# Optimization experiments

Hardware: AMD Instinct MI355X
Metric: run time of the kernel (lower is better)

The kernel has to match this reference:

```python
import jax, jax.numpy as jnp
import numpy as np

B, S, DIM = 2, 2048, 1024
H, DH = 16, 64
WIN = 512


def setup_inputs() -> dict:
    key = jax.random.key(0)
    k1, k2, k3 = jax.random.split(key, 3)
    x = jax.random.normal(k1, (B, S, DIM), dtype=jnp.float32)
    Wqkv = jax.random.normal(k2, (DIM, 3 * H * DH), dtype=jnp.float32) * (DIM ** -0.5)
    Wout = jax.random.normal(k3, (H * DH, DIM), dtype=jnp.float32) * ((H * DH) ** -0.5)
    return {"x": x, "Wqkv": Wqkv, "Wout": Wout}


def reference(x, Wqkv, Wout):
    b, s, _ = x.shape
    qkv = jnp.einsum('bsd,de->bse', x, Wqkv)  # (B,S,3*H*DH)
    q, k, v = jnp.split(qkv, 3, axis=-1)
    # -> (B,H,S,DH)
    q = q.reshape(b, s, H, DH).transpose(0, 2, 1, 3)
    k = k.reshape(b, s, H, DH).transpose(0, 2, 1, 3)
    v = v.reshape(b, s, H, DH).transpose(0, 2, 1, 3)
    scale = DH ** -0.5  # attention sees per-head dim
    scores = jnp.einsum('bhsd,bhtd->bhst', q, k) * scale  # dense (B,H,S,S)
    i = jnp.arange(s)[:, None]
    j = jnp.arange(s)[None, :]
    mask = (j >= i - WIN + 1) & (j <= i)  # causal sliding window
    mask_value = -jnp.finfo(scores.dtype).max
    scores = jnp.where(mask[None, None], scores, mask_value)
    attn = jax.nn.softmax(scores, axis=-1)
    out = jnp.einsum('bhst,bhtd->bhsd', attn, v)
    out = out.transpose(0, 2, 1, 3).reshape(b, s, H * DH)
    return jnp.einsum('bse,ed->bsd', out, Wout)
```

## Files before the change

kernel.cpp:

```cpp
#include <hip/hip_runtime.h>

#define S_LEN 2048
#define BATCH 2
#define HDIM 1024
#define NH 16
#define DH 64
#define WINSZ 512
#define MROWS (BATCH * S_LEN)

typedef __attribute__((ext_vector_type(8))) short bfrag;
typedef __attribute__((ext_vector_type(4))) float f32x4;
typedef __attribute__((ext_vector_type(4))) int i128;

__device__ __forceinline__ short f2bf(float f) {
    union { float f; unsigned u; } v;
    v.f = f;
    unsigned r = v.u + 0x7fffu + ((v.u >> 16) & 1u);
    return (short)(r >> 16);
}

__device__ __forceinline__ void gload_lds16(const short* g, short* l) {
    __builtin_amdgcn_global_load_lds(
        (const __attribute__((address_space(1))) unsigned int*)g,
        (__attribute__((address_space(3))) unsigned int*)l, 16, 0, 0);
}

__global__ __launch_bounds__(256)
void prep_kernel(const float* __restrict__ x, const float* __restrict__ Wqkv,
                 const float* __restrict__ Wout,
                 short* __restrict__ x_bf, short* __restrict__ wqkv_t, short* __restrict__ wout_t)
{
    __shared__ float tile[32][33];
    const int bid = blockIdx.x;
    const int t = threadIdx.x;

    if (bid < 4096) {
        int i = bid * 256 + t;
        float4 v = ((const float4*)x)[i];
        union { short s[4]; int2 p; } u;
        u.s[0] = f2bf(v.x); u.s[1] = f2bf(v.y); u.s[2] = f2bf(v.z); u.s[3] = f2bf(v.w);
        ((int2*)x_bf)[i] = u.p;
        return;
    }

    const float* in;
    short* out;
    int R, C, bx, by;
    if (bid < 7168) {
        int lb = bid - 4096;
        in = Wqkv; out = wqkv_t; R = 1024; C = 3072;
        bx = lb % 96; by = lb / 96;
    } else {
        int lb = bid - 7168;
        in = Wout; out = wout_t; R = 1024; C = 1024;
        bx = lb & 31; by = lb >> 5;
    }
    int tc0 = bx * 32, tr0 = by * 32;
    int c = t & 31, r0 = t >> 5;
    #pragma unroll
    for (int k = 0; k < 4; ++k) {
        int r = r0 + k * 8;
        tile[r][c] = in[(size_t)(tr0 + r) * C + tc0 + c];
    }
    __syncthreads();
    int r2 = t & 31, c0 = t >> 5;
    #pragma unroll
    for (int k = 0; k < 4; ++k) {
        int c2 = c0 + k * 8;
        out[(size_t)(tc0 + c2) * R + tr0 + r2] = f2bf(tile[r2][c2]);
    }
}

__global__ __launch_bounds__(256, 2)
void gemm_qkv(const short* __restrict__ A, const short* __restrict__ Bt,
              short* __restrict__ qk_rm, short* __restrict__ vto)
{
    __shared__ __align__(16) short smraw[17408];
    short (*Al)[4096] = (short(*)[4096])smraw;
    short (*Bl)[4096] = (short(*)[4096])(smraw + 8192);
    const int K = HDIM;
    const int t = threadIdx.x;
    const int lane = t & 63;
    const int wave = t >> 6;
    const int wr = wave >> 1, wc = wave & 1;
    const int m0 = blockIdx.y * 128, n0 = blockIdx.x * 128;
    const int lq = lane & 15;
    const int g = lane >> 4;
    const int lk8 = g << 3;

    f32x4 acc[4][4];
    #pragma unroll
    for (int m = 0; m < 4; ++m)
        #pragma unroll
        for (int n = 0; n < 4; ++n)
            acc[m][n] = (f32x4){0.f, 0.f, 0.f, 0.f};

    const int row0s = t >> 2, col0s = (t & 3) << 3;
    const int row1s = (256 + t) >> 2;
    const size_t dst0 = (size_t)(wave * 64) * 8;
    const size_t dst1 = (size_t)(256 + wave * 64) * 8;

    auto stage = [&](int k0, int sb) {
        gload_lds16(&A[(size_t)(m0 + row0s) * K + k0 + col0s], &Al[sb][0] + dst0);
        gload_lds16(&Bt[(size_t)(n0 + row0s) * K + k0 + col0s], &Bl[sb][0] + dst0);
        gload_lds16(&A[(size_t)(m0 + row1s) * K + k0 + col0s], &Al[sb][0] + dst1);
        gload_lds16(&Bt[(size_t)(n0 + row1s) * K + k0 + col0s], &Bl[sb][0] + dst1);
    };

    const int nk = K >> 5;
    stage(0, 0);
    __syncthreads();
    for (int ki = 0; ki < nk; ++ki) {
        const int cur = ki & 1;
        if (ki + 1 < nk) stage((ki + 1) << 5, cur ^ 1);
        bfrag af[4], bfr[4];
        #pragma unroll
        for (int m = 0; m < 4; ++m)
            af[m] = *(const bfrag*)(&Al[cur][(wr * 64 + m * 16 + lq) * 32 + lk8]);
        #pragma unroll
        for (int n = 0; n < 4; ++n)
            bfr[n] = *(const bfrag*)(&Bl[cur][(wc * 64 + n * 16 + lq) * 32 + lk8]);
        #pragma unroll
        for (int m = 0; m < 4; ++m)
            #pragma unroll
            for (int n = 0; n < 4; ++n)
                acc[m][n] = __builtin_amdgcn_mfma_f32_16x16x32_bf16(af[m], bfr[n], acc[m][n], 0, 0, 0);
        __syncthreads();
    }

    if (n0 < 2048) {
        #pragma unroll
        for (int m = 0; m < 4; ++m)
            #pragma unroll
            for (int n = 0; n < 4; ++n) {
                int col = n0 + wc * 64 + n * 16 + lq;
                int row0 = m0 + wr * 64 + m * 16 + g * 4;
                #pragma unroll
                for (int r = 0; r < 4; ++r)
                    qk_rm[(size_t)(row0 + r) * 2048 + col] = f2bf(acc[m][n][r]);
            }
    } else {
        short* T = smraw;
        #pragma unroll
        for (int m = 0; m < 4; ++m)
            #pragma unroll
            for (int n = 0; n < 4; ++n) {
                int cl = wc * 64 + n * 16 + lq;
                int rl0 = wr * 64 + m * 16 + g * 4;
                union { short sh[4]; int2 w; } u;
                #pragma unroll
                for (int r = 0; r < 4; ++r) u.sh[r] = f2bf(acc[m][n][r]);
                *(int2*)(&T[cl * 136 + rl0]) = u.w;
            }
        __syncthreads();
        const int b = m0 >> 11, sbase = m0 & 2047;
        const int h0 = (n0 - 2048) >> 6;
        #pragma unroll
        for (int i = 0; i < 8; ++i) {
            int c2 = i * 256 + t;
            int rv = c2 >> 4;
            int sc = (c2 & 15) << 3;
            int h = h0 + (rv >> 6), dh = rv & 63;
            i128 v = *(const i128*)(&T[rv * 136 + sc]);
            *(i128*)(&vto[((size_t)((b * NH + h) * DH + dh)) * S_LEN + sbase + sc]) = v;
        }
    }
}

__global__ __launch_bounds__(256, 2)
void gemm_out(const short* __restrict__ A, const short* __restrict__ Bt,
              float* __restrict__ co)
{
    __shared__ __align__(16) short Al[2][128 * 32];
    __shared__ __align__(16) short Bl[2][128 * 32];
    const int K = HDIM, N = HDIM;
    const int t = threadIdx.x;
    const int lane = t & 63;
    const int wave = t >> 6;
    const int wr = wave >> 1, wc = wave & 1;
    const int m0 = blockIdx.y * 128, n0 = blockIdx.x * 128;
    const int lq = lane & 15;
    const int g = lane >> 4;
    const int lk8 = g << 3;

    f32x4 acc[4][4];
    #pragma unroll
    for (int m = 0; m < 4; ++m)
        #pragma unroll
        for (int n = 0; n < 4; ++n)
            acc[m][n] = (f32x4){0.f, 0.f, 0.f, 0.f};

    const int row0s = t >> 2, col0s = (t & 3) << 3;
    const int row1s = (256 + t) >> 2;
    const size_t dst0 = (size_t)(wave * 64) * 8;
    const size_t dst1 = (size_t)(256 + wave * 64) * 8;

    auto stage = [&](int k0, int sb) {
        gload_lds16(&A[(size_t)(m0 + row0s) * K + k0 + col0s], &Al[sb][0] + dst0);
        gload_lds16(&Bt[(size_t)(n0 + row0s) * K + k0 + col0s], &Bl[sb][0] + dst0);
        gload_lds16(&A[(size_t)(m0 + row1s) * K + k0 + col0s], &Al[sb][0] + dst1);
        gload_lds16(&Bt[(size_t)(n0 + row1s) * K + k0 + col0s], &Bl[sb][0] + dst1);
    };

    const int nk = K >> 5;
    stage(0, 0);
    __syncthreads();
    for (int ki = 0; ki < nk; ++ki) {
        const int cur = ki & 1;
        if (ki + 1 < nk) stage((ki + 1) << 5, cur ^ 1);
        bfrag af[4], bfr[4];
        #pragma unroll
        for (int m = 0; m < 4; ++m)
            af[m] = *(const bfrag*)(&Al[cur][(wr * 64 + m * 16 + lq) * 32 + lk8]);
        #pragma unroll
        for (int n = 0; n < 4; ++n)
            bfr[n] = *(const bfrag*)(&Bl[cur][(wc * 64 + n * 16 + lq) * 32 + lk8]);
        #pragma unroll
        for (int m = 0; m < 4; ++m)
            #pragma unroll
            for (int n = 0; n < 4; ++n)
                acc[m][n] = __builtin_amdgcn_mfma_f32_16x16x32_bf16(af[m], bfr[n], acc[m][n], 0, 0, 0);
        __syncthreads();
    }

    #pragma unroll
    for (int m = 0; m < 4; ++m)
        #pragma unroll
        for (int n = 0; n < 4; ++n) {
            int col = n0 + wc * 64 + n * 16 + lq;
            int row0 = m0 + wr * 64 + m * 16 + g * 4;
            #pragma unroll
            for (int r = 0; r < 4; ++r)
                co[(size_t)(row0 + r) * N + col] = acc[m][n][r];
        }
}

__global__ __launch_bounds__(256, 4)
void attn_kernel(const short* __restrict__ qk, const short* __restrict__ vt,
                 short* __restrict__ attno)
{
    __shared__ __align__(16) short Kl[2][64 * 64];
    __shared__ __align__(16) short Vl[2][64 * 64];
    __shared__ __align__(16) short Pl[4][16 * 64];

    const int bid = blockIdx.x;
    const int logical = (bid & 7) * 128 + (bid >> 3);
    const int qblk = logical & 31;
    const int bh = logical >> 5;
    const int b = bh >> 4, h = bh & 15;

    const int t = threadIdx.x;
    const int wave = t >> 6, lane = t & 63;
    const int qb0 = qblk * 64;
    const int i0 = qb0 + wave * 16;
    const short* qbase = qk + (size_t)b * S_LEN * 2048 + h * 64;
    const short* kbase = qk + (size_t)b * S_LEN * 2048 + 1024 + h * 64;
    const short* vp = vt + (size_t)bh * DH * S_LEN;
    char* myP = (char*)&Pl[wave][0];

    const int lq = lane & 15;
    const int g = lane >> 4;
    const int swz = (lq & 7) << 4;
    const int l7 = lq & 7;

    bfrag qf[2];
    qf[0] = *(const bfrag*)(&qbase[(size_t)(i0 + lq) * 2048 + (g << 3)]);
    qf[1] = *(const bfrag*)(&qbase[(size_t)(i0 + lq) * 2048 + 32 + (g << 3)]);

    f32x4 oacc[4];
    #pragma unroll
    for (int d = 0; d < 4; ++d) oacc[d] = (f32x4){0.f, 0.f, 0.f, 0.f};
    float m2 = -1e30f, lrun = 0.f;
    const float QSCALE = 0.125f * 1.44269504f;
    const int qi = i0 + lq;

    int j_lo = qb0 - (WINSZ - 1);
    if (j_lo < 0) j_lo = 0;
    j_lo &= ~63;
    const int nT = ((qb0 + 64) - j_lo) >> 6;

    auto stage = [&](int j0, short* kbuf, short* vbuf) {
        #pragma unroll
        for (int qq = 0; qq < 2; ++qq) {
            int chunk = qq * 256 + wave * 64 + lane;
            int row = chunk >> 3;
            int cc = (chunk & 7) ^ (row & 7);
            short* kdst = kbuf + (size_t)(qq * 256 + wave * 64) * 8;
            short* vdst = vbuf + (size_t)(qq * 256 + wave * 64) * 8;
            gload_lds16(kbase + (size_t)(j_lo + j0 + row) * 2048 + cc * 8, kdst);
            gload_lds16(vp + (size_t)row * S_LEN + j_lo + j0 + cc * 8, vdst);
        }
    };

    stage(0, Kl[0], Vl[0]);
    __syncthreads();

    for (int ti = 0; ti < nT; ++ti) {
        const int cur = ti & 1;
        const int j0 = j_lo + ti * 64;
        if (ti + 1 < nT) stage((ti + 1) * 64, Kl[cur ^ 1], Vl[cur ^ 1]);

        const short* Kc = Kl[cur];
        const short* Vc = Vl[cur];

        f32x4 sc[4];
        __builtin_amdgcn_s_setprio(1);
        #pragma unroll
        for (int tc = 0; tc < 4; ++tc) {
            bfrag a0 = *(const bfrag*)(&Kc[(tc * 16 + lq) * 64 + ((g ^ l7) << 3)]);
            bfrag a1 = *(const bfrag*)(&Kc[(tc * 16 + lq) * 64 + (((4 | g) ^ l7) << 3)]);
            f32x4 z = (f32x4){0.f, 0.f, 0.f, 0.f};
            z = __builtin_amdgcn_mfma_f32_16x16x32_bf16(a0, qf[0], z, 0, 0, 0);
            z = __builtin_amdgcn_mfma_f32_16x16x32_bf16(a1, qf[1], z, 0, 0, 0);
            sc[tc] = z;
        }
        __builtin_amdgcn_s_setprio(0);

        const bool nomask = (j0 >= i0 - (WINSZ - 16)) && (j0 + 63 <= i0);
        float s[4][4];
        float pm = -1e30f;
        #pragma unroll
        for (int tc = 0; tc < 4; ++tc)
            #pragma unroll
            for (int r = 0; r < 4; ++r) {
                float sv = sc[tc][r] * QSCALE;
                if (!nomask) {
                    int kj = j0 + tc * 16 + 4 * g + r;
                    sv = ((kj <= qi) && (kj > qi - WINSZ)) ? sv : -1e30f;
                }
                s[tc][r] = sv;
                pm = fmaxf(pm, sv);
            }
        pm = fmaxf(pm, __shfl_xor(pm, 16));
        pm = fmaxf(pm, __shfl_xor(pm, 32));
        float mnew = fmaxf(m2, pm);
        float scale_old = exp2f(m2 - mnew);
        m2 = mnew;
        float p[4][4];
        float rs = 0.f;
        #pragma unroll
        for (int tc = 0; tc < 4; ++tc)
            #pragma unroll
            for (int r = 0; r < 4; ++r) {
                p[tc][r] = exp2f(s[tc][r] - mnew);
                rs += p[tc][r];
            }
        rs += __shfl_xor(rs, 16);
        rs += __shfl_xor(rs, 32);
        lrun = lrun * scale_old + rs;
        #pragma unroll
        for (int d = 0; d < 4; ++d) {
            f32x4 o = oacc[d];
            o[0] *= scale_old; o[1] *= scale_old; o[2] *= scale_old; o[3] *= scale_old;
            oacc[d] = o;
        }

        #pragma unroll
        for (int tc = 0; tc < 4; ++tc) {
            union { short sh[4]; int2 w; } u;
            u.sh[0] = f2bf(p[tc][0]); u.sh[1] = f2bf(p[tc][1]);
            u.sh[2] = f2bf(p[tc][2]); u.sh[3] = f2bf(p[tc][3]);
            int wb = (lq * 128 + tc * 32 + g * 8) ^ swz;
            *(int2*)(myP + wb) = u.w;
        }
        asm volatile("s_waitcnt lgkmcnt(0)" ::: "memory");

        __builtin_amdgcn_s_setprio(1);
        #pragma unroll
        for (int kt = 0; kt < 2; ++kt) {
            int rb = (lq * 128 + kt * 64 + g * 16) ^ swz;
            bfrag pf = *(const bfrag*)(myP + rb);
            #pragma unroll
            for (int d = 0; d < 4; ++d) {
                bfrag vfr = *(const bfrag*)(&Vc[(d * 16 + lq) * 64 + (((kt * 4 + g) ^ l7) << 3)]);
                oacc[d] = __builtin_amdgcn_mfma_f32_16x16x32_bf16(vfr, pf, oacc[d], 0, 0, 0);
            }
        }
        __builtin_amdgcn_s_setprio(0);
        __syncthreads();
    }

    const float inv_l = 1.f / lrun;
    size_t rowbase = ((size_t)(b * S_LEN + qi)) * HDIM + h * DH;
    #pragma unroll
    for (int d = 0; d < 4; ++d) {
        union { short sh[4]; int2 w; } u;
        #pragma unroll
        for (int r = 0; r < 4; ++r)
            u.sh[r] = f2bf(oacc[d][r] * inv_l);
        *(int2*)(&attno[rowbase + d * 16 + 4 * g]) = u.w;
    }
}

extern "C" void kernel_launch(void* const* d_in, const int* in_sizes, int n_in,
                              void* d_out, int out_size, void* d_ws, size_t ws_size,
                              hipStream_t stream) {
    const float* x = (const float*)d_in[0];
    const float* Wqkv = (const float*)d_in[1];
    const float* Wout = (const float*)d_in[2];
    float* out = (float*)d_out;
    char* ws = (char*)d_ws;

    short* x_bf   = (short*)(ws);
    short* wqkv_t = (short*)(ws + 8388608);
    short* wout_t = (short*)(ws + 14680064);
    short* qk_rm  = (short*)(ws + 16777216);
    short* v_t    = (short*)(ws + 33554432);
    short* attno  = x_bf;

    prep_kernel<<<8192, 256, 0, stream>>>(x, Wqkv, Wout, x_bf, wqkv_t, wout_t);
    gemm_qkv<<<dim3(24, 32), 256, 0, stream>>>(x_bf, wqkv_t, qk_rm, v_t);
    attn_kernel<<<dim3(BATCH * NH * (S_LEN / 64)), 256, 0, stream>>>(qk_rm, v_t, attno);
    gemm_out<<<dim3(8, 32), 256, 0, stream>>>(attno, wout_t, out);
}
```

Measured before the change: 166.6 us.

## Double attention query tile, deepen gemm_out K-step, pack transpose stores

The attention kernel now gives each wave 32 query rows (128 per block), so every staged K/V tile is reused across twice as many queries. The block count halves, occupancy is retuned to 3, and the P buffer doubles. gemm_out stages 64-wide K slices to halve the barrier iterations. The weight transpose writes two bf16 values per 32-bit store, and gemm_qkv launch bounds are raised to 3. The trade-offs are more registers and LDS per block and fewer blocks to fill the GPU.

```diff
diff --git a/kernel.cpp b/kernel.cpp
--- a/kernel.cpp
+++ b/kernel.cpp
@@ -63,15 +63,18 @@
         tile[r][c] = in[(size_t)(tr0 + r) * C + tc0 + c];
     }
     __syncthreads();
-    int r2 = t & 31, c0 = t >> 5;
-    #pragma unroll
-    for (int k = 0; k < 4; ++k) {
-        int c2 = c0 + k * 8;
-        out[(size_t)(tc0 + c2) * R + tr0 + r2] = f2bf(tile[r2][c2]);
-    }
-}
-
-__global__ __launch_bounds__(256, 2)
+    int r2p = (t & 15) << 1, c0 = t >> 4;
+    #pragma unroll
+    for (int k = 0; k < 2; ++k) {
+        int c2 = c0 + k * 16;
+        union { short sh[2]; int w; } u;
+        u.sh[0] = f2bf(tile[r2p][c2]);
+        u.sh[1] = f2bf(tile[r2p + 1][c2]);
+        *(int*)(&out[(size_t)(tc0 + c2) * R + tr0 + r2p]) = u.w;
+    }
+}
+
+__global__ __launch_bounds__(256, 3)
 void gemm_qkv(const short* __restrict__ A, const short* __restrict__ Bt,
               short* __restrict__ qk_rm, short* __restrict__ vto)
 {
@@ -171,8 +174,8 @@
 void gemm_out(const short* __restrict__ A, const short* __restrict__ Bt,
               float* __restrict__ co)
 {
-    __shared__ __align__(16) short Al[2][128 * 32];
-    __shared__ __align__(16) short Bl[2][128 * 32];
+    __shared__ __align__(16) short Al[2][128 * 64];
+    __shared__ __align__(16) short Bl[2][128 * 64];
     const int K = HDIM, N = HDIM;
     const int t = threadIdx.x;
     const int lane = t & 63;
@@ -181,7 +184,6 @@
     const int m0 = blockIdx.y * 128, n0 = blockIdx.x * 128;
     const int lq = lane & 15;
     const int g = lane >> 4;
-    const int lk8 = g << 3;
 
     f32x4 acc[4][4];
     #pragma unroll
@@ -190,36 +192,41 @@
         for (int n = 0; n < 4; ++n)
             acc[m][n] = (f32x4){0.f, 0.f, 0.f, 0.f};
 
-    const int row0s = t >> 2, col0s = (t & 3) << 3;
-    const int row1s = (256 + t) >> 2;
-    const size_t dst0 = (size_t)(wave * 64) * 8;
-    const size_t dst1 = (size_t)(256 + wave * 64) * 8;
-
     auto stage = [&](int k0, int sb) {
-        gload_lds16(&A[(size_t)(m0 + row0s) * K + k0 + col0s], &Al[sb][0] + dst0);
-        gload_lds16(&Bt[(size_t)(n0 + row0s) * K + k0 + col0s], &Bl[sb][0] + dst0);
-        gload_lds16(&A[(size_t)(m0 + row1s) * K + k0 + col0s], &Al[sb][0] + dst1);
-        gload_lds16(&Bt[(size_t)(n0 + row1s) * K + k0 + col0s], &Bl[sb][0] + dst1);
+        #pragma unroll
+        for (int q = 0; q < 4; ++q) {
+            int chunk = q * 256 + t;
+            int row = chunk >> 3, col = (chunk & 7) << 3;
+            size_t dst = (size_t)(q * 256 + wave * 64) * 8;
+            gload_lds16(&A[(size_t)(m0 + row) * K + k0 + col], &Al[sb][0] + dst);
+            gload_lds16(&Bt[(size_t)(n0 + row) * K + k0 + col], &Bl[sb][0] + dst);
+        }
     };
 
-    const int nk = K >> 5;
+    const int nk = K >> 6;
     stage(0, 0);
     __syncthreads();
     for (int ki = 0; ki < nk; ++ki) {
         const int cur = ki & 1;
-        if (ki + 1 < nk) stage((ki + 1) << 5, cur ^ 1);
-        bfrag af[4], bfr[4];
-        #pragma unroll
-        for (int m = 0; m < 4; ++m)
-            af[m] = *(const bfrag*)(&Al[cur][(wr * 64 + m * 16 + lq) * 32 + lk8]);
+        if (ki + 1 < nk) stage((ki + 1) << 6, cur ^ 1);
+        bfrag af[4][2], bfr[4][2];
+        #pragma unroll
+        for (int m = 0; m < 4; ++m)
+            #pragma unroll
+            for (int ks = 0; ks < 2; ++ks)
+                af[m][ks] = *(const bfrag*)(&Al[cur][(wr * 64 + m * 16 + lq) * 64 + ks * 32 + (g << 3)]);
         #pragma unroll
         for (int n = 0; n < 4; ++n)
-            bfr[n] = *(const bfrag*)(&Bl[cur][(wc * 64 + n * 16 + lq) * 32 + lk8]);
-        #pragma unroll
-        for (int m = 0; m < 4; ++m)
-            #pragma unroll
-            for (int n = 0; n < 4; ++n)
-                acc[m][n] = __builtin_amdgcn_mfma_f32_16x16x32_bf16(af[m], bfr[n], acc[m][n], 0, 0, 0);
+            #pragma unroll
+            for (int ks = 0; ks < 2; ++ks)
+                bfr[n][ks] = *(const bfrag*)(&Bl[cur][(wc * 64 + n * 16 + lq) * 64 + ks * 32 + (g << 3)]);
+        #pragma unroll
+        for (int m = 0; m < 4; ++m)
+            #pragma unroll
+            for (int n = 0; n < 4; ++n) {
+                acc[m][n] = __builtin_amdgcn_mfma_f32_16x16x32_bf16(af[m][0], bfr[n][0], acc[m][n], 0, 0, 0);
+                acc[m][n] = __builtin_amdgcn_mfma_f32_16x16x32_bf16(af[m][1], bfr[n][1], acc[m][n], 0, 0, 0);
+            }
         __syncthreads();
     }
 
@@ -235,24 +242,24 @@
         }
 }
 
-__global__ __launch_bounds__(256, 4)
+__global__ __launch_bounds__(256, 3)
 void attn_kernel(const short* __restrict__ qk, const short* __restrict__ vt,
                  short* __restrict__ attno)
 {
     __shared__ __align__(16) short Kl[2][64 * 64];
     __shared__ __align__(16) short Vl[2][64 * 64];
-    __shared__ __align__(16) short Pl[4][16 * 64];
+    __shared__ __align__(16) short Pl[4][32 * 64];
 
     const int bid = blockIdx.x;
-    const int logical = (bid & 7) * 128 + (bid >> 3);
-    const int qblk = logical & 31;
-    const int bh = logical >> 5;
+    const int logical = (bid & 7) * 64 + (bid >> 3);
+    const int qblk = logical & 15;
+    const int bh = logical >> 4;
     const int b = bh >> 4, h = bh & 15;
 
     const int t = threadIdx.x;
     const int wave = t >> 6, lane = t & 63;
-    const int qb0 = qblk * 64;
-    const int i0 = qb0 + wave * 16;
+    const int qb0 = qblk * 128;
+    const int i0 = qb0 + wave * 32;
     const short* qbase = qk + (size_t)b * S_LEN * 2048 + h * 64;
     const short* kbase = qk + (size_t)b * S_LEN * 2048 + 1024 + h * 64;
     const short* vp = vt + (size_t)bh * DH * S_LEN;
@@ -263,32 +270,36 @@
     const int swz = (lq & 7) << 4;
     const int l7 = lq & 7;
 
-    bfrag qf[2];
-    qf[0] = *(const bfrag*)(&qbase[(size_t)(i0 + lq) * 2048 + (g << 3)]);
-    qf[1] = *(const bfrag*)(&qbase[(size_t)(i0 + lq) * 2048 + 32 + (g << 3)]);
-
-    f32x4 oacc[4];
-    #pragma unroll
-    for (int d = 0; d < 4; ++d) oacc[d] = (f32x4){0.f, 0.f, 0.f, 0.f};
-    float m2 = -1e30f, lrun = 0.f;
+    bfrag qf[2][2];
+    #pragma unroll
+    for (int qq = 0; qq < 2; ++qq) {
+        qf[qq][0] = *(const bfrag*)(&qbase[(size_t)(i0 + qq * 16 + lq) * 2048 + (g << 3)]);
+        qf[qq][1] = *(const bfrag*)(&qbase[(size_t)(i0 + qq * 16 + lq) * 2048 + 32 + (g << 3)]);
+    }
+
+    f32x4 oacc[2][4];
+    #pragma unroll
+    for (int qq = 0; qq < 2; ++qq)
+        #pragma unroll
+        for (int d = 0; d < 4; ++d) oacc[qq][d] = (f32x4){0.f, 0.f, 0.f, 0.f};
+    float m2[2] = {-1e30f, -1e30f}, lrun[2] = {0.f, 0.f};
     const float QSCALE = 0.125f * 1.44269504f;
-    const int qi = i0 + lq;
 
     int j_lo = qb0 - (WINSZ - 1);
     if (j_lo < 0) j_lo = 0;
     j_lo &= ~63;
-    const int nT = ((qb0 + 64) - j_lo) >> 6;
-
-    auto stage = [&](int j0, short* kbuf, short* vbuf) {
-        #pragma unroll
-        for (int qq = 0; qq < 2; ++qq) {
-            int chunk = qq * 256 + wave * 64 + lane;
+    const int nT = ((qb0 + 128) - j_lo) >> 6;
+
+    auto stage = [&](int jrel, short* kbuf, short* vbuf) {
+        #pragma unroll
+        for (int qq2 = 0; qq2 < 2; ++qq2) {
+            int chunk = qq2 * 256 + wave * 64 + lane;
             int row = chunk >> 3;
             int cc = (chunk & 7) ^ (row & 7);
-            short* kdst = kbuf + (size_t)(qq * 256 + wave * 64) * 8;
-            short* vdst = vbuf + (size_t)(qq * 256 + wave * 64) * 8;
-            gload_lds16(kbase + (size_t)(j_lo + j0 + row) * 2048 + cc * 8, kdst);
-            gload_lds16(vp + (size_t)row * S_LEN + j_lo + j0 + cc * 8, vdst);
+            short* kdst = kbuf + (size_t)(qq2 * 256 + wave * 64) * 8;
+            short* vdst = vbuf + (size_t)(qq2 * 256 + wave * 64) * 8;
+            gload_lds16(kbase + (size_t)(j_lo + jrel + row) * 2048 + cc * 8, kdst);
+            gload_lds16(vp + (size_t)row * S_LEN + j_lo + jrel + cc * 8, vdst);
         }
     };
 
@@ -303,92 +314,103 @@
         const short* Kc = Kl[cur];
         const short* Vc = Vl[cur];
 
-        f32x4 sc[4];
-        __builtin_amdgcn_s_setprio(1);
-        #pragma unroll
-        for (int tc = 0; tc < 4; ++tc) {
-            bfrag a0 = *(const bfrag*)(&Kc[(tc * 16 + lq) * 64 + ((g ^ l7) << 3)]);
-            bfrag a1 = *(const bfrag*)(&Kc[(tc * 16 + lq) * 64 + (((4 | g) ^ l7) << 3)]);
-            f32x4 z = (f32x4){0.f, 0.f, 0.f, 0.f};
-            z = __builtin_amdgcn_mfma_f32_16x16x32_bf16(a0, qf[0], z, 0, 0, 0);
-            z = __builtin_amdgcn_mfma_f32_16x16x32_bf16(a1, qf[1], z, 0, 0, 0);
-            sc[tc] = z;
-        }
-        __builtin_amdgcn_s_setprio(0);
-
-        const bool nomask = (j0 >= i0 - (WINSZ - 16)) && (j0 + 63 <= i0);
-        float s[4][4];
-        float pm = -1e30f;
-        #pragma unroll
-        for (int tc = 0; tc < 4; ++tc)
-            #pragma unroll
-            for (int r = 0; r < 4; ++r) {
-                float sv = sc[tc][r] * QSCALE;
-                if (!nomask) {
-                    int kj = j0 + tc * 16 + 4 * g + r;
-                    sv = ((kj <= qi) && (kj > qi - WINSZ)) ? sv : -1e30f;
+        #pragma unroll
+        for (int qq = 0; qq < 2; ++qq) {
+            const int i0q = i0 + qq * 16;
+            const int qi = i0q + lq;
+
+            f32x4 sc[4];
+            __builtin_amdgcn_s_setprio(1);
+            #pragma unroll
+            for (int tc = 0; tc < 4; ++tc) {
+                bfrag a0 = *(const bfrag*)(&Kc[(tc * 16 + lq) * 64 + ((g ^ l7) << 3)]);
+                bfrag a1 = *(const bfrag*)(&Kc[(tc * 16 + lq) * 64 + (((4 | g) ^ l7) << 3)]);
+                f32x4 z = (f32x4){0.f, 0.f, 0.f, 0.f};
+                z = __builtin_amdgcn_mfma_f32_16x16x32_bf16(a0, qf[qq][0], z, 0, 0, 0);
+                z = __builtin_amdgcn_mfma_f32_16x16x32_bf16(a1, qf[qq][1], z, 0, 0, 0);
+                sc[tc] = z;
+            }
+            __builtin_amdgcn_s_setprio(0);
+
+            const bool nomask = (j0 >= i0q - (WINSZ - 16)) && (j0 + 63 <= i0q);
+            float s[4][4];
+            float pm = -1e30f;
+            #pragma unroll
+            for (int tc = 0; tc < 4; ++tc)
+                #pragma unroll
+                for (int r = 0; r < 4; ++r) {
+                    float sv = sc[tc][r] * QSCALE;
+                    if (!nomask) {
+                        int kj = j0 + tc * 16 + 4 * g + r;
+                        sv = ((kj <= qi) && (kj > qi - WINSZ)) ? sv : -1e30f;
+                    }
+                    s[tc][r] = sv;
+                    pm = fmaxf(pm, sv);
                 }
-                s[tc][r] = sv;
-                pm = fmaxf(pm, sv);
-            }
-        pm = fmaxf(pm, __shfl_xor(pm, 16));
-        pm = fmaxf(pm, __shfl_xor(pm, 32));
-        float mnew = fmaxf(m2, pm);
-        float scale_old = exp2f(m2 - mnew);
-        m2 = mnew;
-        float p[4][4];
-        float rs = 0.f;
-        #pragma unroll
-        for (int tc = 0; tc < 4; ++tc)
-            #pragma unroll
-            for (int r = 0; r < 4; ++r) {
-                p[tc][r] = exp2f(s[tc][r] - mnew);
-                rs += p[tc][r];
-            }
-        rs += __shfl_xor(rs, 16);
-        rs += __shfl_xor(rs, 32);
-        lrun = lrun * scale_old + rs;
+            pm = fmaxf(pm, __shfl_xor(pm, 16));
+            pm = fmaxf(pm, __shfl_xor(pm, 32));
+            float mnew = fmaxf(m2[qq], pm);
+            float scale_old = exp2f(m2[qq] - mnew);
+            m2[qq] = mnew;
+            float p[4][4];
+            float rs = 0.f;
+            #pragma unroll
+            for (int tc = 0; tc < 4; ++tc)
+                #pragma unroll
+                for (int r = 0; r < 4; ++r) {
+                    p[tc][r] = exp2f(s[tc][r] - mnew);
+                    rs += p[tc][r];
+                }
+            rs += __shfl_xor(rs, 16);
+            rs += __shfl_xor(rs, 32);
+            lrun[qq] = lrun[qq] * scale_old + rs;
+            #pragma unroll
+            for (int d = 0; d < 4; ++d) {
+                f32x4 o = oacc[qq][d];
+                o[0] *= scale_old; o[1] *= scale_old; o[2] *= scale_old; o[3] *= scale_old;
+                oacc[qq][d] = o;
+            }
+
+            char* myPq = myP + qq * 2048;
+            #pragma unroll
+            for (int tc = 0; tc < 4; ++tc) {
+                union { short sh[4]; int2 w; } u;
+                u.sh[0] = f2bf(p[tc][0]); u.sh[1] = f2bf(p[tc][1]);
+                u.sh[2] = f2bf(p[tc][2]); u.sh[3] = f2bf(p[tc][3]);
+                int wb = (lq * 128 + tc * 32 + g * 8) ^ swz;
+                *(int2*)(myPq + wb) = u.w;
+            }
+            asm volatile("s_waitcnt lgkmcnt(0)" ::: "memory");
+
+            __builtin_amdgcn_s_setprio(1);
+            #pragma unroll
+            for (int kt = 0; kt < 2; ++kt) {
+                int rb = (lq * 128 + kt * 64 + g * 16) ^ swz;
+                bfrag pf = *(const bfrag*)(myPq + rb);
+                #pragma unroll
+                for (int d = 0; d < 4; ++d) {
+                    bfrag vfr = *(const bfrag*)(&Vc[(d * 16 + lq) * 64 + (((kt * 4 + g) ^ l7) << 3)]);
+                    oacc[qq][d] = __builtin_amdgcn_mfma_f32_16x16x32_bf16(vfr, pf, oacc[qq][d], 0, 0, 0);
+                }
+            }
+            __builtin_amdgcn_s_setprio(0);
+        }
+        __syncthreads();
+    }
+
+    #pragma unroll
+    for (int qq = 0; qq < 2; ++qq) {
+        const float inv_l = 1.f / lrun[qq];
+        const int qi = i0 + qq * 16 + lq;
+        size_t rowbase = ((size_t)(b * S_LEN + qi)) * HDIM + h * DH;
         #pragma unroll
         for (int d = 0; d < 4; ++d) {
-            f32x4 o = oacc[d];
-            o[0] *= scale_old; o[1] *= scale_old; o[2] *= scale_old; o[3] *= scale_old;
-            oacc[d] = o;
-        }
-
-        #pragma unroll
-        for (int tc = 0; tc < 4; ++tc) {
             union { short sh[4]; int2 w; } u;
-            u.sh[0] = f2bf(p[tc][0]); u.sh[1] = f2bf(p[tc][1]);
-            u.sh[2] = f2bf(p[tc][2]); u.sh[3] = f2bf(p[tc][3]);
-            int wb = (lq * 128 + tc * 32 + g * 8) ^ swz;
-            *(int2*)(myP + wb) = u.w;
-        }
-        asm volatile("s_waitcnt lgkmcnt(0)" ::: "memory");
-
-        __builtin_amdgcn_s_setprio(1);
-        #pragma unroll
-        for (int kt = 0; kt < 2; ++kt) {
-            int rb = (lq * 128 + kt * 64 + g * 16) ^ swz;
-            bfrag pf = *(const bfrag*)(myP + rb);
-            #pragma unroll
-            for (int d = 0; d < 4; ++d) {
-                bfrag vfr = *(const bfrag*)(&Vc[(d * 16 + lq) * 64 + (((kt * 4 + g) ^ l7) << 3)]);
-                oacc[d] = __builtin_amdgcn_mfma_f32_16x16x32_bf16(vfr, pf, oacc[d], 0, 0, 0);
-            }
-        }
-        __builtin_amdgcn_s_setprio(0);
-        __syncthreads();
-    }
-
-    const float inv_l = 1.f / lrun;
-    size_t rowbase = ((size_t)(b * S_LEN + qi)) * HDIM + h * DH;
-    #pragma unroll
-    for (int d = 0; d < 4; ++d) {
-        union { short sh[4]; int2 w; } u;
-        #pragma unroll
-        for (int r = 0; r < 4; ++r)
-            u.sh[r] = f2bf(oacc[d][r] * inv_l);
-        *(int2*)(&attno[rowbase + d * 16 + 4 * g]) = u.w;
+            #pragma unroll
+            for (int r = 0; r < 4; ++r)
+                u.sh[r] = f2bf(oacc[qq][d][r] * inv_l);
+            *(int2*)(&attno[rowbase + d * 16 + 4 * g]) = u.w;
+        }
     }
 }
 
@@ -410,6 +432,6 @@
 
     prep_kernel<<<8192, 256, 0, stream>>>(x, Wqkv, Wout, x_bf, wqkv_t, wout_t);
     gemm_qkv<<<dim3(24, 32), 256, 0, stream>>>(x_bf, wqkv_t, qk_rm, v_t);
-    attn_kernel<<<dim3(BATCH * NH * (S_LEN / 64)), 256, 0, stream>>>(qk_rm, v_t, attno);
+    attn_kernel<<<dim3(BATCH * NH * (S_LEN / 128)), 256, 0, stream>>>(qk_rm, v_t, attno);
     gemm_out<<<dim3(8, 32), 256, 0, stream>>>(attno, wout_t, out);
 }
```

Result: slower. 175.8 us (+5.5%).
